# Kernel tuning notes

Measured on AMD Instinct MI355X. Metric: run time of the kernel, lower is better.

Reference implementation:

```python
import jax, jax.numpy as jnp
import numpy as np

N_NODES = 100000
N_EDGES = 1600000
IN_CH, HID_CH, OUT_CH = 128, 128, 64


def _glorot(key, shape):
    lim = np.sqrt(6.0 / (shape[0] + shape[1])).astype(np.float32)
    return jax.random.uniform(key, shape, jnp.float32, -lim, lim)


def setup_inputs() -> dict:
    key = jax.random.key(0)
    ks = jax.random.split(key, 11)
    x = jax.random.normal(ks[0], (N_NODES, IN_CH), jnp.float32)
    edge_index = jax.random.randint(ks[1], (2, N_EDGES), 0, N_NODES, dtype=jnp.int64)
    dims = [(IN_CH, HID_CH), (HID_CH, HID_CH), (HID_CH, OUT_CH)]
    params = {}
    for i, (din, dout) in enumerate(dims):
        params[f"Wl{i}"] = _glorot(ks[2 + 3 * i], (din, dout))
        params[f"Wr{i}"] = _glorot(ks[3 + 3 * i], (din, dout))
        params[f"b{i}"] = jnp.zeros((dout,), jnp.float32)
    return {"x": x, "edge_index": edge_index, **params}


def _sage_conv(x, src, dst, Wl, Wr, b):
    # mean aggregation of neighbor (source) features at each destination node
    msg_sum = jax.ops.segment_sum(x[src], dst, num_segments=N_NODES)  # [N, din]
    deg = jax.ops.segment_sum(jnp.ones((src.shape[0],), x.dtype), dst,
                              num_segments=N_NODES)
    mean = msg_sum / jnp.maximum(deg, 1.0)[:, None]
    # lin_l(aggr) + lin_r(self), bias only in lin_l (PyG SAGEConv default)
    return mean @ Wl + x @ Wr + b


def reference(x, edge_index, Wl0, Wr0, b0, Wl1, Wr1, b1, Wl2, Wr2, b2):
    src, dst = edge_index[0], edge_index[1]
    h = jax.nn.relu(_sage_conv(x, src, dst, Wl0, Wr0, b0))  # dropout = identity (eval)
    h = jax.nn.relu(_sage_conv(h, src, dst, Wl1, Wr1, b1))
    out = _sage_conv(h, src, dst, Wl2, Wr2, b2)
    return out
```

## Files before the change

### kernel.cpp

```cpp
#include <hip/hip_runtime.h>
#include <stdint.h>

#define NN 100000
#define NE 1600000
#define NBUK 782
#define G 256
#define CHUNK 6250

typedef unsigned int u32;
typedef unsigned short u16;
typedef short v8s __attribute__((ext_vector_type(8)));
typedef float v4f __attribute__((ext_vector_type(4)));

union U4S8 {
    uint4 u;
    v8s s;
};

__device__ __forceinline__ float bf2f(u16 u) {
    return __uint_as_float(((u32)u) << 16);
}
__device__ __forceinline__ u16 f2bf(float f) {
    u32 u = __float_as_uint(f);
    u = u + 0x7FFFu + ((u >> 16) & 1u);
    return (u16)(u >> 16);
}
__device__ __forceinline__ float lo16(u32 u) { return __uint_as_float(u << 16); }
__device__ __forceinline__ float hi16(u32 u) {
    return __uint_as_float(u & 0xFFFF0000u);
}

__global__ void detect_kernel(const u32* __restrict__ ei,
                              const u32* __restrict__ x, int* flags) {
    __shared__ int bad64, badbf;
    int t = threadIdx.x;
    if (t == 0) { bad64 = 0; badbf = 0; }
    __syncthreads();
    if (ei[2 * t + 1] != 0u) atomicAdd(&bad64, 1);
    u32 d = x[t];
    u32 e = (d >> 7) & 0xFFu;
    if (e != 0u && (e < 96u || e > 160u)) atomicAdd(&badbf, 1);
    __syncthreads();
    if (t == 0) {
        flags[0] = (bad64 < 16) ? 1 : 0;
        flags[1] = (badbf < 16) ? 1 : 0;
    }
}

__global__ void conv_x(const void* __restrict__ x, const int* __restrict__ flags,
                       u32* __restrict__ xb, u32* __restrict__ h1,
                       u32* __restrict__ h2) {
    int i = blockIdx.x * 256 + threadIdx.x;
    if (i >= NN * 64) {
        int p = i - NN * 64;
        if (p < 64) {
            xb[NN * 64 + p] = 0;
            h1[NN * 64 + p] = 0;
            h2[NN * 64 + p] = 0;
        }
        return;
    }
    u32 o;
    if (flags[1]) {
        o = ((const u32*)x)[i];
    } else {
        float2 v = ((const float2*)x)[i];
        o = ((u32)f2bf(v.y) << 16) | (u32)f2bf(v.x);
    }
    xb[i] = o;
}

__global__ void wt_prep_all(const void* __restrict__ Wr0,
                            const void* __restrict__ Wl0,
                            const void* __restrict__ b0,
                            const void* __restrict__ Wr1,
                            const void* __restrict__ Wl1,
                            const void* __restrict__ b1,
                            const void* __restrict__ Wr2,
                            const void* __restrict__ Wl2,
                            const void* __restrict__ b2,
                            const int* __restrict__ flags,
                            u16* __restrict__ WT0, float* __restrict__ bf0,
                            u16* __restrict__ WT1, float* __restrict__ bf1,
                            u16* __restrict__ WT2, float* __restrict__ bf2_) {
    const void* Wr;
    const void* Wl;
    const void* bias;
    u16* WT;
    float* bias_f;
    int cout, t;
    if (blockIdx.x < 128) {
        Wr = Wr0; Wl = Wl0; bias = b0; WT = WT0; bias_f = bf0; cout = 128;
        t = blockIdx.x * 256 + threadIdx.x;
    } else if (blockIdx.x < 256) {
        Wr = Wr1; Wl = Wl1; bias = b1; WT = WT1; bias_f = bf1; cout = 128;
        t = (blockIdx.x - 128) * 256 + threadIdx.x;
    } else {
        Wr = Wr2; Wl = Wl2; bias = b2; WT = WT2; bias_f = bf2_; cout = 64;
        t = (blockIdx.x - 256) * 256 + threadIdx.x;
    }
    if (t < 256 * cout) {
        int k = t / cout, c = t % cout;
        const void* W = (k < 128) ? Wr : Wl;
        int kk = k & 127;
        float v;
        if (flags[1])
            v = bf2f(((const u16*)W)[kk * cout + c]);
        else
            v = ((const float*)W)[kk * cout + c];
        WT[c * 256 + k] = f2bf(v);
    }
    if (t < cout) {
        bias_f[t] =
            flags[1] ? bf2f(((const u16*)bias)[t]) : ((const float*)bias)[t];
    }
}

__global__ __launch_bounds__(256) void p1_hist(const void* __restrict__ ei,
                                               const int* __restrict__ flags,
                                               int* __restrict__ hist) {
    __shared__ int h[NBUK];
    int g = blockIdx.x, t = threadIdx.x;
    for (int b = t; b < NBUK; b += 256) h[b] = 0;
    __syncthreads();
    int e0 = g * CHUNK;
    int e1 = e0 + CHUNK;
    const int* p = (const int*)ei;
    if (flags[0]) {
        for (int e = e0 + t; e < e1; e += 256)
            atomicAdd(&h[p[2 * (NE + e)] >> 7], 1);
    } else {
        for (int e = e0 + t; e < e1; e += 256)
            atomicAdd(&h[p[NE + e] >> 7], 1);
    }
    __syncthreads();
    for (int b = t; b < NBUK; b += 256) hist[b * G + g] = h[b];
}

__global__ void scan_block_g(const int* __restrict__ in, int* __restrict__ out,
                             int* __restrict__ bsums, int n) {
    __shared__ int sS[256];
    int t = threadIdx.x;
    int base = blockIdx.x * 1024 + t * 4;
    int c[4];
#pragma unroll
    for (int i = 0; i < 4; ++i) c[i] = (base + i < n) ? in[base + i] : 0;
    int s = c[0] + c[1] + c[2] + c[3];
    sS[t] = s;
    __syncthreads();
    for (int dlt = 1; dlt < 256; dlt <<= 1) {
        int v = (t >= dlt) ? sS[t - dlt] : 0;
        __syncthreads();
        sS[t] += v;
        __syncthreads();
    }
    int run = sS[t] - s;
    if (t == 255) bsums[blockIdx.x] = sS[255];
#pragma unroll
    for (int i = 0; i < 4; ++i) {
        if (base + i < n) out[base + i] = run;
        run += c[i];
    }
}

__global__ void scan_top_g(int* bsums, int nb) {
    __shared__ int sS[256];
    int t = threadIdx.x;
    int v = (t < nb) ? bsums[t] : 0;
    sS[t] = v;
    __syncthreads();
    for (int d = 1; d < 256; d <<= 1) {
        int u = (t >= d) ? sS[t - d] : 0;
        __syncthreads();
        sS[t] += u;
        __syncthreads();
    }
    if (t < nb) bsums[t] = sS[t] - v;
}

__global__ void scan_add_g(int* __restrict__ out, const int* __restrict__ bsums,
                           int n) {
    int i = blockIdx.x * 256 + threadIdx.x;
    if (i < n) out[i] += bsums[i >> 10];
}

__global__ __launch_bounds__(256) void p2_scatter(const void* __restrict__ ei,
                                                  const int* __restrict__ flags,
                                                  const int* __restrict__ histS,
                                                  int2* __restrict__ ebuf) {
    __shared__ int cur[NBUK];
    int g = blockIdx.x, t = threadIdx.x;
    for (int b = t; b < NBUK; b += 256) cur[b] = histS[b * G + g];
    __syncthreads();
    int e0 = g * CHUNK;
    int e1 = e0 + CHUNK;
    const int* p = (const int*)ei;
    int is64 = flags[0];
    for (int e = e0 + t; e < e1; e += 256) {
        int s, d;
        if (is64) {
            s = p[2 * e];
            d = p[2 * (NE + e)];
        } else {
            s = p[e];
            d = p[NE + e];
        }
        int pos = atomicAdd(&cur[d >> 7], 1);
        ebuf[pos] = make_int2(s, d);
    }
}

__global__ __launch_bounds__(256) void p3_build(const int* __restrict__ histS,
                                                const int2* __restrict__ ebuf,
                                                int* __restrict__ off,
                                                int* __restrict__ ssrc) {
    __shared__ int cnt[128], pref[128], cur[128];
    int b = blockIdx.x, t = threadIdx.x;
    int node0 = b << 7;
    int bs = histS[b * G];
    int be = (b == NBUK - 1) ? NE : histS[(b + 1) * G];
    if (t < 128) cnt[t] = 0;
    __syncthreads();
    for (int e = bs + t; e < be; e += 256)
        atomicAdd(&cnt[ebuf[e].y - node0], 1);
    __syncthreads();
    if (t < 128) pref[t] = cnt[t];
    __syncthreads();
    for (int d = 1; d < 128; d <<= 1) {
        int v = 0;
        if (t < 128 && t >= d) v = pref[t - d];
        __syncthreads();
        if (t < 128) pref[t] += v;
        __syncthreads();
    }
    if (t < 128) {
        int ex = pref[t] - cnt[t];
        cur[t] = ex;
        int node = node0 + t;
        if (node < NN) off[node] = bs + ex;
    }
    if (b == NBUK - 1 && t == 0) off[NN] = NE;
    __syncthreads();
    for (int e = bs + t; e < be; e += 256) {
        int2 sd = ebuf[e];
        int pos = atomicAdd(&cur[sd.y - node0], 1);
        ssrc[bs + pos] = sd.x;
    }
}

__global__ __launch_bounds__(256) void gather_mean_b(
    const u32* __restrict__ feat, const int* __restrict__ off,
    const int* __restrict__ ssrc, u32* __restrict__ meanB) {
    int node = blockIdx.x * 4 + (threadIdx.x >> 6);
    int lane = threadIdx.x & 63;
    int o0 = __builtin_amdgcn_readfirstlane(off[node]);
    int o1 = __builtin_amdgcn_readfirstlane(off[node + 1]);
    int cnt = o1 - o0;
    float a0 = 0.f, a1 = 0.f;
    for (int base = 0; base < cnt; base += 64) {
        int lim = cnt - base;
        if (lim > 64) lim = 64;
        int myidx = (lane < lim) ? ssrc[o0 + base + lane] : NN;
        int jb = (lim + 15) & ~15;
        for (int j = 0; j < jb; j += 16) {
            u32 uu[16];
#pragma unroll
            for (int q = 0; q < 16; ++q) {
                int sidx = __builtin_amdgcn_readlane(myidx, j + q);
                uu[q] = feat[(size_t)sidx * 64 + lane];
            }
#pragma unroll
            for (int q = 0; q < 16; ++q) {
                a0 += lo16(uu[q]);
                a1 += hi16(uu[q]);
            }
        }
    }
    float inv = 1.0f / (float)(cnt > 0 ? cnt : 1);
    meanB[node * 64 + lane] =
        ((u32)f2bf(a1 * inv) << 16) | (u32)f2bf(a0 * inv);
}

template <int COUT, bool RELU, bool FINAL>
__global__ __launch_bounds__(256) void sage_mfma(
    const u16* __restrict__ selfB, const u16* __restrict__ meanB,
    const u16* __restrict__ WT, const float* __restrict__ bias_f,
    void* __restrict__ out, const int* __restrict__ flags) {
    constexpr int NT = COUT / 16;
    const int tid = threadIdx.x;
    const int wave = tid >> 6;
    const int lane = tid & 63;
    const int n16 = lane & 15;
    const int quad = lane >> 4;
    const int rowbase = blockIdx.x * 128 + wave * 32;
    const int bfin = flags[1];

    int ar0 = rowbase + n16;
    int ar1 = rowbase + 16 + n16;
    ar0 = (ar0 < NN) ? ar0 : (NN - 1);
    ar1 = (ar1 < NN) ? ar1 : (NN - 1);

    const u16* aS0 = selfB + (size_t)ar0 * 128 + quad * 8;
    const u16* aS1 = selfB + (size_t)ar1 * 128 + quad * 8;
    const u16* aM0 = meanB + (size_t)ar0 * 128 + quad * 8;
    const u16* aM1 = meanB + (size_t)ar1 * 128 + quad * 8;
    const u16* bp = WT + (size_t)n16 * 256 + quad * 8;

    v4f acc[2][NT];
#pragma unroll
    for (int mt = 0; mt < 2; ++mt)
#pragma unroll
        for (int nt = 0; nt < NT; ++nt) acc[mt][nt] = (v4f)(0.f);

#pragma unroll
    for (int ks = 0; ks < 8; ++ks) {
        const int ko = (ks & 3) * 32;
        U4S8 a0, a1;
        a0.u = *(const uint4*)((ks < 4 ? aS0 : aM0) + ko);
        a1.u = *(const uint4*)((ks < 4 ? aS1 : aM1) + ko);
        U4S8 b[NT];
#pragma unroll
        for (int nt = 0; nt < NT; ++nt)
            b[nt].u = *(const uint4*)(bp + nt * 16 * 256 + ks * 32);
#pragma unroll
        for (int nt = 0; nt < NT; ++nt) {
            acc[0][nt] = __builtin_amdgcn_mfma_f32_16x16x32_bf16(
                a0.s, b[nt].s, acc[0][nt], 0, 0, 0);
            acc[1][nt] = __builtin_amdgcn_mfma_f32_16x16x32_bf16(
                a1.s, b[nt].s, acc[1][nt], 0, 0, 0);
        }
    }

#pragma unroll
    for (int nt = 0; nt < NT; ++nt) {
        const int c = nt * 16 + n16;
        const float bv = bias_f[c];
#pragma unroll
        for (int mt = 0; mt < 2; ++mt) {
#pragma unroll
            for (int r = 0; r < 4; ++r) {
                int row = rowbase + mt * 16 + quad * 4 + r;
                if (row < NN) {
                    float v = acc[mt][nt][r] + bv;
                    if (RELU) v = fmaxf(v, 0.f);
                    if (FINAL && !bfin)
                        ((float*)out)[(size_t)row * COUT + c] = v;
                    else
                        ((u16*)out)[(size_t)row * COUT + c] = f2bf(v);
                }
            }
        }
    }
}

extern "C" void kernel_launch(void* const* d_in, const int* in_sizes, int n_in,
                              void* d_out, int out_size, void* d_ws,
                              size_t ws_size, hipStream_t stream) {
    const void* x = d_in[0];
    const void* ei = d_in[1];
    const void* Wl0 = d_in[2];
    const void* Wr0 = d_in[3];
    const void* b0 = d_in[4];
    const void* Wl1 = d_in[5];
    const void* Wr1 = d_in[6];
    const void* b1 = d_in[7];
    const void* Wl2 = d_in[8];
    const void* Wr2 = d_in[9];
    const void* b2 = d_in[10];

    char* ws = (char*)d_ws;
    size_t o = 0;
    auto alloc = [&](size_t bytes) {
        void* p = ws + o;
        o = (o + bytes + 511) & ~(size_t)511;
        return p;
    };
    int* flags = (int*)alloc(16);
    int* hist = (int*)alloc((size_t)NBUK * G * 4);
    int* bsums = (int*)alloc(256 * 4);
    int* off = (int*)alloc((NN + 1) * 4);
    int* ssrc = (int*)alloc((size_t)NE * 4);
    int2* ebuf = (int2*)alloc((size_t)NE * 8);
    u32* xb = (u32*)alloc((size_t)(NN + 1) * 64 * 4);
    u32* meanB = (u32*)alloc((size_t)NN * 64 * 4);
    u32* h1 = (u32*)alloc((size_t)(NN + 1) * 64 * 4);
    u32* h2 = (u32*)alloc((size_t)(NN + 1) * 64 * 4);
    u16* WT0 = (u16*)alloc(256 * 128 * 2);
    u16* WT1 = (u16*)alloc(256 * 128 * 2);
    u16* WT2 = (u16*)alloc(256 * 64 * 2);
    float* bf0 = (float*)alloc(128 * 4);
    float* bf1 = (float*)alloc(128 * 4);
    float* bf2_ = (float*)alloc(64 * 4);

    constexpr int L = NBUK * G;
    constexpr int NBLK = (L + 1023) / 1024;
    constexpr int RB = (NN + 127) / 128;

    detect_kernel<<<1, 256, 0, stream>>>((const u32*)ei, (const u32*)x, flags);
    conv_x<<<(NN * 64 + 64 + 255) / 256, 256, 0, stream>>>(x, flags, xb, h1,
                                                           h2);
    wt_prep_all<<<320, 256, 0, stream>>>(Wr0, Wl0, b0, Wr1, Wl1, b1, Wr2, Wl2,
                                         b2, flags, WT0, bf0, WT1, bf1, WT2,
                                         bf2_);

    p1_hist<<<G, 256, 0, stream>>>(ei, flags, hist);
    scan_block_g<<<NBLK, 256, 0, stream>>>(hist, hist, bsums, L);
    scan_top_g<<<1, 256, 0, stream>>>(bsums, NBLK);
    scan_add_g<<<(L + 255) / 256, 256, 0, stream>>>(hist, bsums, L);
    p2_scatter<<<G, 256, 0, stream>>>(ei, flags, hist, ebuf);
    p3_build<<<NBUK, 256, 0, stream>>>(hist, ebuf, off, ssrc);

    gather_mean_b<<<NN / 4, 256, 0, stream>>>(xb, off, ssrc, meanB);
    sage_mfma<128, true, false><<<RB, 256, 0, stream>>>(
        (const u16*)xb, (const u16*)meanB, WT0, bf0, h1, flags);
    gather_mean_b<<<NN / 4, 256, 0, stream>>>(h1, off, ssrc, meanB);
    sage_mfma<128, true, false><<<RB, 256, 0, stream>>>(
        (const u16*)h1, (const u16*)meanB, WT1, bf1, h2, flags);
    gather_mean_b<<<NN / 4, 256, 0, stream>>>(h2, off, ssrc, meanB);
    sage_mfma<64, false, true><<<RB, 256, 0, stream>>>(
        (const u16*)h2, (const u16*)meanB, WT2, bf2_, d_out, flags);
}
```

Baseline: 475.2 us.

## Shrink sage_mfma tile to 16 rows per wave and preload A operands

Each wave in the dense SAGE MFMA kernel now handles 16 rows instead of 32, giving twice as many blocks. All eight A fragments (self and mean) are loaded up front and the loop runs over output tiles, fetching the B slices for each tile. A launch-bounds occupancy hint is added. The aim is more parallelism and occupancy to hide memory latency. The cost is that B weights are reused across half as many rows, so weight traffic through cache roughly doubles.

```diff
diff --git a/kernel.cpp b/kernel.cpp
--- a/kernel.cpp
+++ b/kernel.cpp
@@ -282,7 +282,7 @@
 }
 
 template <int COUT, bool RELU, bool FINAL>
-__global__ __launch_bounds__(256) void sage_mfma(
+__global__ __launch_bounds__(256, 4) void sage_mfma(
     const u16* __restrict__ selfB, const u16* __restrict__ meanB,
     const u16* __restrict__ WT, const float* __restrict__ bias_f,
     void* __restrict__ out, const int* __restrict__ flags) {
@@ -292,43 +292,37 @@
     const int lane = tid & 63;
     const int n16 = lane & 15;
     const int quad = lane >> 4;
-    const int rowbase = blockIdx.x * 128 + wave * 32;
+    const int rowbase = blockIdx.x * 64 + wave * 16;
     const int bfin = flags[1];
 
-    int ar0 = rowbase + n16;
-    int ar1 = rowbase + 16 + n16;
-    ar0 = (ar0 < NN) ? ar0 : (NN - 1);
-    ar1 = (ar1 < NN) ? ar1 : (NN - 1);
-
-    const u16* aS0 = selfB + (size_t)ar0 * 128 + quad * 8;
-    const u16* aS1 = selfB + (size_t)ar1 * 128 + quad * 8;
-    const u16* aM0 = meanB + (size_t)ar0 * 128 + quad * 8;
-    const u16* aM1 = meanB + (size_t)ar1 * 128 + quad * 8;
+    int ar = rowbase + n16;
+    ar = (ar < NN) ? ar : (NN - 1);
+
+    const u16* aS = selfB + (size_t)ar * 128 + quad * 8;
+    const u16* aM = meanB + (size_t)ar * 128 + quad * 8;
     const u16* bp = WT + (size_t)n16 * 256 + quad * 8;
 
-    v4f acc[2][NT];
-#pragma unroll
-    for (int mt = 0; mt < 2; ++mt)
-#pragma unroll
-        for (int nt = 0; nt < NT; ++nt) acc[mt][nt] = (v4f)(0.f);
-
-#pragma unroll
-    for (int ks = 0; ks < 8; ++ks) {
-        const int ko = (ks & 3) * 32;
-        U4S8 a0, a1;
-        a0.u = *(const uint4*)((ks < 4 ? aS0 : aM0) + ko);
-        a1.u = *(const uint4*)((ks < 4 ? aS1 : aM1) + ko);
-        U4S8 b[NT];
-#pragma unroll
-        for (int nt = 0; nt < NT; ++nt)
-            b[nt].u = *(const uint4*)(bp + nt * 16 * 256 + ks * 32);
-#pragma unroll
-        for (int nt = 0; nt < NT; ++nt) {
-            acc[0][nt] = __builtin_amdgcn_mfma_f32_16x16x32_bf16(
-                a0.s, b[nt].s, acc[0][nt], 0, 0, 0);
-            acc[1][nt] = __builtin_amdgcn_mfma_f32_16x16x32_bf16(
-                a1.s, b[nt].s, acc[1][nt], 0, 0, 0);
-        }
+    U4S8 a[8];
+#pragma unroll
+    for (int ks = 0; ks < 4; ++ks) {
+        a[ks].u = *(const uint4*)(aS + ks * 32);
+        a[4 + ks].u = *(const uint4*)(aM + ks * 32);
+    }
+
+    v4f acc[NT];
+#pragma unroll
+    for (int nt = 0; nt < NT; ++nt) acc[nt] = (v4f)(0.f);
+
+#pragma unroll
+    for (int nt = 0; nt < NT; ++nt) {
+        U4S8 b[8];
+#pragma unroll
+        for (int ks = 0; ks < 8; ++ks)
+            b[ks].u = *(const uint4*)(bp + nt * 16 * 256 + ks * 32);
+#pragma unroll
+        for (int ks = 0; ks < 8; ++ks)
+            acc[nt] = __builtin_amdgcn_mfma_f32_16x16x32_bf16(a[ks].s, b[ks].s,
+                                                              acc[nt], 0, 0, 0);
     }
 
 #pragma unroll
@@ -336,18 +330,15 @@
         const int c = nt * 16 + n16;
         const float bv = bias_f[c];
 #pragma unroll
-        for (int mt = 0; mt < 2; ++mt) {
-#pragma unroll
-            for (int r = 0; r < 4; ++r) {
-                int row = rowbase + mt * 16 + quad * 4 + r;
-                if (row < NN) {
-                    float v = acc[mt][nt][r] + bv;
-                    if (RELU) v = fmaxf(v, 0.f);
-                    if (FINAL && !bfin)
-                        ((float*)out)[(size_t)row * COUT + c] = v;
-                    else
-                        ((u16*)out)[(size_t)row * COUT + c] = f2bf(v);
-                }
+        for (int r = 0; r < 4; ++r) {
+            int row = rowbase + quad * 4 + r;
+            if (row < NN) {
+                float v = acc[nt][r] + bv;
+                if (RELU) v = fmaxf(v, 0.f);
+                if (FINAL && !bfin)
+                    ((float*)out)[(size_t)row * COUT + c] = v;
+                else
+                    ((u16*)out)[(size_t)row * COUT + c] = f2bf(v);
             }
         }
     }
@@ -394,7 +385,7 @@
 
     constexpr int L = NBUK * G;
     constexpr int NBLK = (L + 1023) / 1024;
-    constexpr int RB = (NN + 127) / 128;
+    constexpr int RB64 = (NN + 63) / 64;
 
     detect_kernel<<<1, 256, 0, stream>>>((const u32*)ei, (const u32*)x, flags);
     conv_x<<<(NN * 64 + 64 + 255) / 256, 256, 0, stream>>>(x, flags, xb, h1,
@@ -411,12 +402,12 @@
     p3_build<<<NBUK, 256, 0, stream>>>(hist, ebuf, off, ssrc);
 
     gather_mean_b<<<NN / 4, 256, 0, stream>>>(xb, off, ssrc, meanB);
-    sage_mfma<128, true, false><<<RB, 256, 0, stream>>>(
+    sage_mfma<128, true, false><<<RB64, 256, 0, stream>>>(
         (const u16*)xb, (const u16*)meanB, WT0, bf0, h1, flags);
     gather_mean_b<<<NN / 4, 256, 0, stream>>>(h1, off, ssrc, meanB);
-    sage_mfma<128, true, false><<<RB, 256, 0, stream>>>(
+    sage_mfma<128, true, false><<<RB64, 256, 0, stream>>>(
         (const u16*)h1, (const u16*)meanB, WT1, bf1, h2, flags);
     gather_mean_b<<<NN / 4, 256, 0, stream>>>(h2, off, ssrc, meanB);
-    sage_mfma<64, false, true><<<RB, 256, 0, stream>>>(
+    sage_mfma<64, false, true><<<RB64, 256, 0, stream>>>(
         (const u16*)h2, (const u16*)meanB, WT2, bf2_, d_out, flags);
 }
```

After: 513.8 us. 8.1% more time.
